# Kernel optimization log

Measured on AMD Instinct MI355X. Metric: run time of the kernel, lower is better.

The kernel has to match this reference:

```python
import jax, jax.numpy as jnp
import numpy as np

D_FEATURE = 1024
HEAD = 16
D_K = 64
D_V = 64
EPS = 1e-6


def setup_inputs() -> dict:
    key = jax.random.key(0)
    ks = jax.random.split(key, 12)
    B, S = 2, 2048
    s_in = 1.0 / np.sqrt(D_FEATURE)
    s_o = 1.0 / np.sqrt(HEAD * D_V)
    return {
        "q": jax.random.normal(ks[0], (B, S, D_FEATURE), jnp.float32),
        "k": jax.random.normal(ks[1], (B, S, D_FEATURE), jnp.float32),
        "v": jax.random.normal(ks[2], (B, S, D_FEATURE), jnp.float32),
        "Wq": jax.random.uniform(ks[3], (D_FEATURE, HEAD * D_K), jnp.float32, -s_in, s_in),
        "bq": jnp.zeros((HEAD * D_K,), jnp.float32),
        "Wk": jax.random.uniform(ks[4], (D_FEATURE, HEAD * D_K), jnp.float32, -s_in, s_in),
        "bk": jnp.zeros((HEAD * D_K,), jnp.float32),
        "Wv": jax.random.uniform(ks[5], (D_FEATURE, HEAD * D_V), jnp.float32, -s_in, s_in),
        "bv": jnp.zeros((HEAD * D_V,), jnp.float32),
        "Wo": jax.random.uniform(ks[6], (HEAD * D_V, D_FEATURE), jnp.float32, -s_o, s_o),
        "bo": jnp.zeros((D_FEATURE,), jnp.float32),
        "gamma": jnp.ones((D_FEATURE,), jnp.float32),
        "beta": jnp.zeros((D_FEATURE,), jnp.float32),
    }


def reference(q, k, v, Wq, bq, Wk, bk, Wv, bv, Wo, bo, gamma, beta):
    B, Sq, _ = q.shape
    Sk, Sv = k.shape[1], v.shape[1]
    shortcut = v
    # projections -> (b, h, s, d)
    qh = (q @ Wq + bq).reshape(B, Sq, HEAD, D_K).transpose(0, 2, 1, 3)
    kh = (k @ Wk + bk).reshape(B, Sk, HEAD, D_K).transpose(0, 2, 1, 3)
    vh = (v @ Wv + bv).reshape(B, Sv, HEAD, D_V).transpose(0, 2, 1, 3)
    scale = 1.0 / np.sqrt(D_K).astype(np.float32)
    scores = jnp.einsum('bhqd,bhkd->bhqk', qh * scale, kh)
    attn = jax.nn.softmax(scores, axis=-1)  # dropout is identity (p=0 / eval)
    ctx = jnp.einsum('bhqk,bhkd->bhqd', attn, vh)
    ctx = ctx.transpose(0, 2, 1, 3).reshape(B, Sv, HEAD * D_V)
    out = ctx @ Wo + bo
    out = out + shortcut
    # LayerNorm, eps=1e-6
    mu = out.mean(-1, keepdims=True)
    var = out.var(-1, keepdims=True)
    out = (out - mu) * jax.lax.rsqrt(var + EPS) * gamma + beta
    return out
```

## Files before the change

kernel.cpp:

```cpp
#include <hip/hip_runtime.h>

#define D_FEAT 1024
#define NTOK   4096
#define SEQ    2048
#define NHEAD  16
#define DK     64
#define QSCALE 0.1803368801111204f

typedef float          f32x4  __attribute__((ext_vector_type(4)));
typedef float          f32x16 __attribute__((ext_vector_type(16)));
typedef short          s16x8  __attribute__((ext_vector_type(8)));
typedef unsigned short u16x4  __attribute__((ext_vector_type(4)));

__device__ __forceinline__ unsigned short f2bf(float f) {
  union { float f; unsigned int u; } x; x.f = f;
  unsigned int r = x.u + 0x7fffu + ((x.u >> 16) & 1u);
  return (unsigned short)(r >> 16);
}
__device__ __forceinline__ unsigned short f2h(float f) {
  union { _Float16 h; unsigned short u; } x; x.h = (_Float16)f; return x.u;
}
__device__ __forceinline__ float h2f(unsigned short u) {
  union { _Float16 h; unsigned short u; } x; x.u = u; return (float)x.h;
}

__device__ __forceinline__ f32x4 mfma16(s16x8 a, s16x8 b, f32x4 c) {
  return __builtin_amdgcn_mfma_f32_16x16x32_bf16(a, b, c, 0, 0, 0);
}
__device__ __forceinline__ f32x16 mfma32(s16x8 a, s16x8 b, f32x16 c) {
  return __builtin_amdgcn_mfma_f32_32x32x16_bf16(a, b, c, 0, 0, 0);
}

__device__ __forceinline__ void gload16(const void* g, void* l) {
  __builtin_amdgcn_global_load_lds(
      (const __attribute__((address_space(1))) void*)g,
      (__attribute__((address_space(3))) void*)l, 16, 0, 0);
}

__global__ __launch_bounds__(256) void prep_kernel(
    const float* __restrict__ q, const float* __restrict__ k, const float* __restrict__ v,
    const float* __restrict__ Wq, const float* __restrict__ Wk,
    const float* __restrict__ Wv, const float* __restrict__ Wo,
    unsigned short* __restrict__ qb, unsigned short* __restrict__ kb,
    unsigned short* __restrict__ vb,
    unsigned short* __restrict__ WT, unsigned short* __restrict__ Wot)
{
  __shared__ float tile[32][33];
  const int bx = blockIdx.x, tid = threadIdx.x;
  if (bx < 12288) {
    int sel = bx >> 12;
    const float* src = sel == 0 ? q : (sel == 1 ? k : v);
    unsigned short* dst = sel == 0 ? qb : (sel == 1 ? kb : vb);
    size_t i = ((size_t)(bx & 4095) * 256 + tid) * 4;
    float4 f = *(const float4*)(src + i);
    u16x4 o; o.x = f2bf(f.x); o.y = f2bf(f.y); o.z = f2bf(f.z); o.w = f2bf(f.w);
    *(u16x4*)(dst + i) = o;
  } else {
    int t = bx - 12288;
    int z = t >> 10, rest = t & 1023;
    int bxt = rest & 31, byt = rest >> 5;
    const float* W = z == 0 ? Wq : z == 1 ? Wk : z == 2 ? Wv : Wo;
    unsigned short* T = (z < 3) ? (WT + (size_t)z * 1024 * 1024) : Wot;
    int tx = tid & 31, ty = tid >> 5;
    int n = bxt * 32 + tx;
    for (int i = 0; i < 4; ++i) {
      int kk = byt * 32 + ty + i * 8;
      tile[ty + i * 8][tx] = W[(size_t)kk * D_FEAT + n];
    }
    __syncthreads();
    int kk = byt * 32 + tx;
    for (int i = 0; i < 4; ++i) {
      int n2 = bxt * 32 + ty + i * 8;
      T[(size_t)n2 * D_FEAT + kk] = f2bf(tile[tx][ty + i * 8]);
    }
  }
}

__global__ __launch_bounds__(256, 3) void gemm_qkv(
    const unsigned short* __restrict__ qb, const unsigned short* __restrict__ kb,
    const unsigned short* __restrict__ vb, const unsigned short* __restrict__ WT,
    const float* __restrict__ bq, const float* __restrict__ bk, const float* __restrict__ bv,
    unsigned short* __restrict__ Qp, unsigned short* __restrict__ Kp, unsigned short* __restrict__ Vt)
{
  __shared__ __align__(16) unsigned short sAB[2 * 128 * 64];
  unsigned short* sA = sAB;
  unsigned short* sB = sAB + 128 * 64;
  const int tid = threadIdx.x;
  const int wave = tid >> 6, lane = tid & 63;
  const int quad = lane >> 4, l16 = lane & 15;
  const int wx = wave & 1, wy = wave >> 1;

  const int blk = blockIdx.x;
  const int xcd = blk & 7, jj = blk >> 3;
  const int chunk = jj >> 5;
  const int rest = jj & 31;
  const int n0i = rest & 7;
  const int by  = xcd * 4 + (rest >> 3);

  const unsigned short* rA;
  const unsigned short* rB;
  int m0, n0;
  if (chunk < 2) {
    m0 = by * 128; n0 = n0i * 128;
    rA = (chunk ? kb : qb) + (size_t)m0 * D_FEAT;
    rB = WT + (size_t)(chunk * 1024 + n0) * D_FEAT;
  } else {
    m0 = n0i * 128; n0 = by * 128;
    rA = WT + (size_t)(2048 + m0) * D_FEAT;
    rB = vb + (size_t)n0 * D_FEAT;
  }

  f32x4 acc[4][4];
  for (int mt = 0; mt < 4; ++mt)
    for (int nt = 0; nt < 4; ++nt) acc[mt][nt] = (f32x4){0.f, 0.f, 0.f, 0.f};

  const int rw8 = lane >> 3;
  const int cls = ((lane & 7) ^ (lane >> 3)) * 8;
  const int sw = l16 & 7;

  for (int k0 = 0; k0 < D_FEAT; k0 += 64) {
    __syncthreads();
    for (int j = 0; j < 4; ++j) {
      int ch = wave * 4 + j;
      gload16(rA + (size_t)(ch * 8 + rw8) * D_FEAT + k0 + cls, sA + ch * 512);
      gload16(rB + (size_t)(ch * 8 + rw8) * D_FEAT + k0 + cls, sB + ch * 512);
    }
    __syncthreads();
    s16x8 af[2][4], bfr[2][4];
    for (int kk = 0; kk < 2; ++kk) {
      int c = ((kk * 4 + quad) ^ sw) * 8;
      for (int mt = 0; mt < 4; ++mt)
        af[kk][mt] = *(const s16x8*)(sA + (wy * 64 + mt * 16 + l16) * 64 + c);
      for (int nt = 0; nt < 4; ++nt)
        bfr[kk][nt] = *(const s16x8*)(sB + (wx * 64 + nt * 16 + l16) * 64 + c);
    }
    for (int kk = 0; kk < 2; ++kk)
      for (int mt = 0; mt < 4; ++mt)
        for (int nt = 0; nt < 4; ++nt)
          acc[mt][nt] = mfma16(af[kk][mt], bfr[kk][nt], acc[mt][nt]);
  }

  if (chunk < 2) {
    const float* bias = chunk ? bk : bq;
    unsigned short* Cp = chunk ? Kp : Qp;
    const float scale = chunk == 0 ? QSCALE : 1.0f;
    for (int mt = 0; mt < 4; ++mt)
      for (int nt = 0; nt < 4; ++nt) {
        int col = n0 + wx * 64 + nt * 16 + l16;
        float bcol = bias[col];
        for (int r = 0; r < 4; ++r) {
          int row = m0 + wy * 64 + mt * 16 + quad * 4 + r;
          Cp[(size_t)row * D_FEAT + col] = f2bf((acc[mt][nt][r] + bcol) * scale);
        }
      }
  } else {
    for (int mt = 0; mt < 4; ++mt)
      for (int r = 0; r < 4; ++r) {
        float bfeat = bv[m0 + wy * 64 + mt * 16 + quad * 4 + r];
        for (int nt = 0; nt < 4; ++nt) acc[mt][nt][r] += bfeat;
      }
    unsigned short* tb = sAB;
    for (int p = 0; p < 2; ++p) {
      __syncthreads();
      if (wx == p) {
        for (int mt = 0; mt < 4; ++mt)
          for (int nt = 0; nt < 4; ++nt) {
            int tok_loc = nt * 16 + l16;
            for (int r = 0; r < 4; ++r) {
              int f_loc = wy * 64 + mt * 16 + quad * 4 + r;
              tb[f_loc * 72 + tok_loc] = f2bf(acc[mt][nt][r]);
            }
          }
      }
      __syncthreads();
      int n_base = n0 + p * 64;
      int b = n_base >> 11, tok0 = n_base & 2047;
      int ck = lane & 7;
      for (int j = 0; j < 4; ++j) {
        int f_loc = (wave * 4 + j) * 8 + rw8;
        int f = m0 + f_loc, hh = f >> 6, dv = f & 63;
        *(s16x8*)(Vt + ((size_t)(b * 16 + hh) * 64 + dv) * SEQ + tok0 + ck * 8) =
            *(const s16x8*)(tb + f_loc * 72 + ck * 8);
      }
    }
  }
}

__global__ __launch_bounds__(256) void gemm_o(
    const unsigned short* __restrict__ A, const unsigned short* __restrict__ Bt,
    const float* __restrict__ bias, const float* __restrict__ resid,
    float* __restrict__ Cout)
{
  __shared__ __align__(16) unsigned short sA[128 * 64];
  __shared__ __align__(16) unsigned short sB[64 * 64];
  const int tid = threadIdx.x;
  const int wave = tid >> 6, lane = tid & 63;
  const int quad = lane >> 4, l16 = lane & 15;
  const int wx = wave & 1, wy = wave >> 1;

  const int blk = blockIdx.x;
  const int xcd = blk & 7, jj = blk >> 3;
  const int n0 = (jj & 15) * 64;
  const int m0 = (xcd * 4 + (jj >> 4)) * 128;

  f32x4 acc[4][2];
  for (int mt = 0; mt < 4; ++mt)
    for (int nt = 0; nt < 2; ++nt) acc[mt][nt] = (f32x4){0.f, 0.f, 0.f, 0.f};

  const int rw8 = lane >> 3;
  const int cls = ((lane & 7) ^ (lane >> 3)) * 8;
  const int sw = l16 & 7;

  for (int k0 = 0; k0 < D_FEAT; k0 += 64) {
    __syncthreads();
    for (int j = 0; j < 4; ++j) {
      int ch = wave * 4 + j;
      gload16(A + (size_t)(m0 + ch * 8 + rw8) * D_FEAT + k0 + cls, sA + ch * 512);
    }
    for (int j = 0; j < 2; ++j) {
      int ch = wave * 2 + j;
      gload16(Bt + (size_t)(n0 + ch * 8 + rw8) * D_FEAT + k0 + cls, sB + ch * 512);
    }
    __syncthreads();
    s16x8 af[2][4], bfr[2][2];
    for (int kk = 0; kk < 2; ++kk) {
      int c = ((kk * 4 + quad) ^ sw) * 8;
      for (int mt = 0; mt < 4; ++mt)
        af[kk][mt] = *(const s16x8*)(sA + (wy * 64 + mt * 16 + l16) * 64 + c);
      for (int nt = 0; nt < 2; ++nt)
        bfr[kk][nt] = *(const s16x8*)(sB + (wx * 32 + nt * 16 + l16) * 64 + c);
    }
    for (int kk = 0; kk < 2; ++kk)
      for (int mt = 0; mt < 4; ++mt)
        for (int nt = 0; nt < 2; ++nt)
          acc[mt][nt] = mfma16(af[kk][mt], bfr[kk][nt], acc[mt][nt]);
  }

  for (int mt = 0; mt < 4; ++mt)
    for (int nt = 0; nt < 2; ++nt) {
      int col = n0 + wx * 32 + nt * 16 + l16;
      float bcol = bias[col];
      for (int r = 0; r < 4; ++r) {
        int row = m0 + wy * 64 + mt * 16 + quad * 4 + r;
        Cout[(size_t)row * D_FEAT + col] =
            acc[mt][nt][r] + bcol + resid[(size_t)row * D_FEAT + col];
      }
    }
}

__global__ __launch_bounds__(256, 4) void flash_part(
    const unsigned short* __restrict__ Qp,
    const unsigned short* __restrict__ Kp,
    const unsigned short* __restrict__ Vt,
    unsigned short* __restrict__ Opart,
    float* __restrict__ L)
{
  __shared__ __align__(16) unsigned short sQ[128 * 64];
  __shared__ __align__(16) unsigned short sK[64 * 64];
  __shared__ __align__(16) unsigned short sV[64 * 64];

  const int tid = threadIdx.x;
  const int wave = tid >> 6, lane = tid & 63;
  const int l32 = lane & 31, h = lane >> 5;

  const int blk = blockIdx.x;
  const int xcd = blk & 7, jj = blk >> 3;
  const int grp = xcd * 8 + (jj >> 4);
  const int q0 = (jj & 15) * 128;
  const int bh = grp & 31, z = grp >> 5;
  const int b = bh >> 4, hd = bh & 15;
  const int kbase = z * (SEQ / 2);
  const size_t base = (size_t)b * SEQ * D_FEAT + (size_t)hd * DK;
  const unsigned short* vt = Vt + (size_t)bh * 64 * SEQ;

  const int rw8 = lane >> 3;
  const int cls = ((lane & 7) ^ (lane >> 3)) * 8;

  for (int j = 0; j < 4; ++j) {
    int ch = wave * 4 + j;
    gload16(Qp + base + (size_t)(q0 + ch * 8 + rw8) * D_FEAT + cls, sQ + ch * 512);
  }
  __syncthreads();

  const int qrow = wave * 32 + l32;
  const int qsw = qrow & 7;
  s16x8 bq[4];
  for (int s = 0; s < 4; ++s)
    bq[s] = *(const s16x8*)(sQ + qrow * 64 + ((2 * s + h) ^ qsw) * 8);

  unsigned short* sP = sQ;

  f32x16 o0, o1;
  for (int r = 0; r < 16; ++r) { o0[r] = 0.f; o1[r] = 0.f; }
  float lsum = 0.f;

  const int ksw0 = l32 & 7;

  for (int k0 = kbase; k0 < kbase + SEQ / 2; k0 += 64) {
    __syncthreads();
    for (int j = 0; j < 2; ++j) {
      int ch = wave * 2 + j;
      gload16(Kp + base + (size_t)(k0 + ch * 8 + rw8) * D_FEAT + cls, sK + ch * 512);
      gload16(vt + (size_t)(ch * 8 + rw8) * SEQ + k0 + cls, sV + ch * 512);
    }
    __syncthreads();

    f32x16 st0, st1;
    for (int r = 0; r < 16; ++r) { st0[r] = 0.f; st1[r] = 0.f; }
    for (int s = 0; s < 4; ++s) {
      int csw = ((2 * s + h) ^ ksw0) * 8;
      s16x8 a0 = *(const s16x8*)(sK + l32 * 64 + csw);
      s16x8 a1 = *(const s16x8*)(sK + (32 + l32) * 64 + csw);
      st0 = mfma32(a0, bq[s], st0);
      st1 = mfma32(a1, bq[s], st1);
    }

    const int rowb = qrow * 64;
    for (int g = 0; g < 4; ++g) {
      unsigned int u[4];
      for (int r = 0; r < 4; ++r) {
        union { float f; unsigned int v; } x;
        x.f = __builtin_exp2f(st0[4 * g + r]);
        lsum += x.f; u[r] = x.v;
      }
      unsigned int w0 = __builtin_amdgcn_perm(u[1], u[0], 0x07060302u);
      unsigned int w1 = __builtin_amdgcn_perm(u[3], u[2], 0x07060302u);
      *(uint2*)(sP + rowb + ((g ^ qsw) * 8) + 4 * h) = make_uint2(w0, w1);
    }
    for (int g = 0; g < 4; ++g) {
      unsigned int u[4];
      for (int r = 0; r < 4; ++r) {
        union { float f; unsigned int v; } x;
        x.f = __builtin_exp2f(st1[4 * g + r]);
        lsum += x.f; u[r] = x.v;
      }
      unsigned int w0 = __builtin_amdgcn_perm(u[1], u[0], 0x07060302u);
      unsigned int w1 = __builtin_amdgcn_perm(u[3], u[2], 0x07060302u);
      *(uint2*)(sP + rowb + (((4 + g) ^ qsw) * 8) + 4 * h) = make_uint2(w0, w1);
    }

    s16x8 bp[4];
    for (int s = 0; s < 4; ++s)
      bp[s] = *(const s16x8*)(sP + rowb + ((2 * s + h) ^ qsw) * 8);

    for (int s = 0; s < 4; ++s) {
      int csw = ((2 * s + h) ^ ksw0) * 8;
      s16x8 a0 = *(const s16x8*)(sV + l32 * 64 + csw);
      s16x8 a1 = *(const s16x8*)(sV + (32 + l32) * 64 + csw);
      o0 = mfma32(a0, bp[s], o0);
      o1 = mfma32(a1, bp[s], o1);
    }
  }

  lsum += __shfl_xor(lsum, 32, 64);
  const size_t trow = (size_t)(z * 32 + bh) * SEQ + (q0 + qrow);
  unsigned short* orow = Opart + trow * 64;
  for (int g = 0; g < 4; ++g) {
    u16x4 ov;
    for (int r = 0; r < 4; ++r) ov[r] = f2h(o0[4 * g + r]);
    *(u16x4*)(orow + 8 * g + 4 * h) = ov;
  }
  for (int g = 0; g < 4; ++g) {
    u16x4 ov;
    for (int r = 0; r < 4; ++r) ov[r] = f2h(o1[4 * g + r]);
    *(u16x4*)(orow + 32 + 8 * g + 4 * h) = ov;
  }
  if (h == 0) L[trow] = lsum;
}

__global__ __launch_bounds__(256) void combine_kernel(
    const unsigned short* __restrict__ Opart, const float* __restrict__ L,
    unsigned short* __restrict__ ctx)
{
  const int idx = blockIdx.x * 256 + threadIdx.x;
  const int dq = idx & 15;
  const int trow = idx >> 4;
  const int bh = trow >> 11, tok = trow & 2047;
  const int b = bh >> 4, h = bh & 15;
  const int HS = 32 * SEQ;

  float inv = __builtin_amdgcn_rcpf(L[trow] + L[HS + trow]);

  u16x4 p0 = *(const u16x4*)(Opart + (size_t)trow * 64 + dq * 4);
  u16x4 p1 = *(const u16x4*)(Opart + ((size_t)HS + trow) * 64 + dq * 4);
  u16x4 o;
  for (int r = 0; r < 4; ++r)
    o[r] = f2bf((h2f(p0[r]) + h2f(p1[r])) * inv);
  *(u16x4*)(ctx + (size_t)b * SEQ * D_FEAT + (size_t)tok * D_FEAT + h * 64 + dq * 4) = o;
}

__global__ __launch_bounds__(256) void ln_kernel(
    const float* __restrict__ x, const float* __restrict__ gamma,
    const float* __restrict__ beta, float* __restrict__ out)
{
  const int row = blockIdx.x, tid = threadIdx.x;
  const int wave = tid >> 6, lane = tid & 63;
  const float* xr = x + (size_t)row * D_FEAT;
  float4 v = ((const float4*)xr)[tid];
  float s  = v.x + v.y + v.z + v.w;
  float ss = v.x * v.x + v.y * v.y + v.z * v.z + v.w * v.w;
  for (int off = 1; off < 64; off <<= 1) {
    s  += __shfl_xor(s,  off, 64);
    ss += __shfl_xor(ss, off, 64);
  }
  __shared__ float red[8];
  if (lane == 0) { red[wave] = s; red[wave + 4] = ss; }
  __syncthreads();
  s  = red[0] + red[1] + red[2] + red[3];
  ss = red[4] + red[5] + red[6] + red[7];
  float mean = s * (1.f / D_FEAT);
  float var  = ss * (1.f / D_FEAT) - mean * mean;
  float rstd = rsqrtf(var + 1e-6f);
  float4 g  = ((const float4*)gamma)[tid];
  float4 bt = ((const float4*)beta)[tid];
  float4 o;
  o.x = (v.x - mean) * rstd * g.x + bt.x;
  o.y = (v.y - mean) * rstd * g.y + bt.y;
  o.z = (v.z - mean) * rstd * g.z + bt.z;
  o.w = (v.w - mean) * rstd * g.w + bt.w;
  ((float4*)(out + (size_t)row * D_FEAT))[tid] = o;
}

extern "C" void kernel_launch(void* const* d_in, const int* in_sizes, int n_in,
                              void* d_out, int out_size, void* d_ws, size_t ws_size,
                              hipStream_t stream) {
  const float* q     = (const float*)d_in[0];
  const float* k     = (const float*)d_in[1];
  const float* v     = (const float*)d_in[2];
  const float* Wq    = (const float*)d_in[3];
  const float* bq    = (const float*)d_in[4];
  const float* Wk    = (const float*)d_in[5];
  const float* bk    = (const float*)d_in[6];
  const float* Wv    = (const float*)d_in[7];
  const float* bv    = (const float*)d_in[8];
  const float* Wo    = (const float*)d_in[9];
  const float* bo    = (const float*)d_in[10];
  const float* gamma = (const float*)d_in[11];
  const float* beta  = (const float*)d_in[12];

  char* w = (char*)d_ws;
  const size_t MB = 1u << 20;
  unsigned short* qb    = (unsigned short*)(w + 0 * MB);
  unsigned short* kb    = (unsigned short*)(w + 8 * MB);
  unsigned short* vb    = (unsigned short*)(w + 16 * MB);
  unsigned short* WT    = (unsigned short*)(w + 24 * MB);
  unsigned short* Wot   = (unsigned short*)(w + 30 * MB);
  unsigned short* Qp    = (unsigned short*)(w + 32 * MB);
  unsigned short* Kp    = (unsigned short*)(w + 40 * MB);
  unsigned short* Vt    = (unsigned short*)(w + 48 * MB);
  unsigned short* ctx   = (unsigned short*)(w + 56 * MB);
  float*          tmp   = (float*)(w + 64 * MB);
  unsigned short* Opart = (unsigned short*)(w + 0 * MB);
  float*          L     = (float*)(w + 16 * MB);

  prep_kernel<<<16384, 256, 0, stream>>>(q, k, v, Wq, Wk, Wv, Wo, qb, kb, vb, WT, Wot);

  gemm_qkv<<<768, 256, 0, stream>>>(qb, kb, vb, WT, bq, bk, bv, Qp, Kp, Vt);

  flash_part<<<1024, 256, 0, stream>>>(Qp, Kp, Vt, Opart, L);

  combine_kernel<<<4096, 256, 0, stream>>>(Opart, L, ctx);

  gemm_o<<<512, 256, 0, stream>>>(ctx, Wot, bo, v, tmp);

  ln_kernel<<<NTOK, 256, 0, stream>>>(tmp, gamma, beta, (float*)d_out);
}
```

Before: 246.4 us.

## Fuse all six stages into one persistent kernel with grid barriers

Replaces six separate launches (prep, QKV GEMM, flash attention, combine, output GEMM, LayerNorm) with a single persistent kernel of 1024 blocks. The stages are separated by atomic-counter grid barriers. The aim is to remove per-launch overhead and inter-kernel gaps. The costs are idle blocks in stages that use fewer than 1024 blocks, and a forward-progress requirement that all 1024 blocks be co-resident (occupancy hint of 4 per CU). Buffer offsets are reused (tmp now aliases Qp/Kp), and the weight transpose store is vectorised.

```diff
diff --git a/kernel.cpp b/kernel.cpp
--- a/kernel.cpp
+++ b/kernel.cpp
@@ -6,6 +6,7 @@
 #define NHEAD  16
 #define DK     64
 #define QSCALE 0.1803368801111204f
+#define GRID   1024
 
 typedef float          f32x4  __attribute__((ext_vector_type(4)));
 typedef float          f32x16 __attribute__((ext_vector_type(16)));
@@ -37,388 +38,373 @@
       (__attribute__((address_space(3))) void*)l, 16, 0, 0);
 }
 
-__global__ __launch_bounds__(256) void prep_kernel(
+__device__ __forceinline__ void gbar(unsigned* cnt, unsigned target) {
+  __syncthreads();
+  if (threadIdx.x == 0) {
+    __threadfence();
+    atomicAdd(cnt, 1u);
+    while (atomicAdd(cnt, 0u) < target) __builtin_amdgcn_s_sleep(2);
+    __threadfence();
+  }
+  __syncthreads();
+}
+
+__global__ __launch_bounds__(256, 4) void mega_kernel(
     const float* __restrict__ q, const float* __restrict__ k, const float* __restrict__ v,
     const float* __restrict__ Wq, const float* __restrict__ Wk,
     const float* __restrict__ Wv, const float* __restrict__ Wo,
-    unsigned short* __restrict__ qb, unsigned short* __restrict__ kb,
-    unsigned short* __restrict__ vb,
-    unsigned short* __restrict__ WT, unsigned short* __restrict__ Wot)
+    const float* __restrict__ bq, const float* __restrict__ bk,
+    const float* __restrict__ bv, const float* __restrict__ bo,
+    const float* __restrict__ gamma, const float* __restrict__ beta,
+    unsigned short* qb, unsigned short* kb, unsigned short* vb,
+    unsigned short* WT, unsigned short* Wot,
+    unsigned short* Qp, unsigned short* Kp, unsigned short* Vt,
+    unsigned short* Opart, float* L, unsigned short* ctx, float* tmp,
+    float* out, unsigned* bar)
 {
-  __shared__ float tile[32][33];
-  const int bx = blockIdx.x, tid = threadIdx.x;
-  if (bx < 12288) {
-    int sel = bx >> 12;
-    const float* src = sel == 0 ? q : (sel == 1 ? k : v);
-    unsigned short* dst = sel == 0 ? qb : (sel == 1 ? kb : vb);
-    size_t i = ((size_t)(bx & 4095) * 256 + tid) * 4;
-    float4 f = *(const float4*)(src + i);
-    u16x4 o; o.x = f2bf(f.x); o.y = f2bf(f.y); o.z = f2bf(f.z); o.w = f2bf(f.w);
-    *(u16x4*)(dst + i) = o;
-  } else {
-    int t = bx - 12288;
-    int z = t >> 10, rest = t & 1023;
-    int bxt = rest & 31, byt = rest >> 5;
-    const float* W = z == 0 ? Wq : z == 1 ? Wk : z == 2 ? Wv : Wo;
-    unsigned short* T = (z < 3) ? (WT + (size_t)z * 1024 * 1024) : Wot;
-    int tx = tid & 31, ty = tid >> 5;
-    int n = bxt * 32 + tx;
-    for (int i = 0; i < 4; ++i) {
-      int kk = byt * 32 + ty + i * 8;
-      tile[ty + i * 8][tx] = W[(size_t)kk * D_FEAT + n];
-    }
-    __syncthreads();
-    int kk = byt * 32 + tx;
-    for (int i = 0; i < 4; ++i) {
-      int n2 = bxt * 32 + ty + i * 8;
-      T[(size_t)n2 * D_FEAT + kk] = f2bf(tile[tx][ty + i * 8]);
-    }
-  }
-}
-
-__global__ __launch_bounds__(256, 3) void gemm_qkv(
-    const unsigned short* __restrict__ qb, const unsigned short* __restrict__ kb,
-    const unsigned short* __restrict__ vb, const unsigned short* __restrict__ WT,
-    const float* __restrict__ bq, const float* __restrict__ bk, const float* __restrict__ bv,
-    unsigned short* __restrict__ Qp, unsigned short* __restrict__ Kp, unsigned short* __restrict__ Vt)
-{
-  __shared__ __align__(16) unsigned short sAB[2 * 128 * 64];
-  unsigned short* sA = sAB;
-  unsigned short* sB = sAB + 128 * 64;
+  __shared__ __align__(16) unsigned char smem[32768];
   const int tid = threadIdx.x;
+  const int blk = blockIdx.x;
   const int wave = tid >> 6, lane = tid & 63;
   const int quad = lane >> 4, l16 = lane & 15;
-  const int wx = wave & 1, wy = wave >> 1;
-
-  const int blk = blockIdx.x;
-  const int xcd = blk & 7, jj = blk >> 3;
-  const int chunk = jj >> 5;
-  const int rest = jj & 31;
-  const int n0i = rest & 7;
-  const int by  = xcd * 4 + (rest >> 3);
-
-  const unsigned short* rA;
-  const unsigned short* rB;
-  int m0, n0;
-  if (chunk < 2) {
-    m0 = by * 128; n0 = n0i * 128;
-    rA = (chunk ? kb : qb) + (size_t)m0 * D_FEAT;
-    rB = WT + (size_t)(chunk * 1024 + n0) * D_FEAT;
-  } else {
-    m0 = n0i * 128; n0 = by * 128;
-    rA = WT + (size_t)(2048 + m0) * D_FEAT;
-    rB = vb + (size_t)n0 * D_FEAT;
-  }
-
-  f32x4 acc[4][4];
-  for (int mt = 0; mt < 4; ++mt)
-    for (int nt = 0; nt < 4; ++nt) acc[mt][nt] = (f32x4){0.f, 0.f, 0.f, 0.f};
-
   const int rw8 = lane >> 3;
   const int cls = ((lane & 7) ^ (lane >> 3)) * 8;
-  const int sw = l16 & 7;
-
-  for (int k0 = 0; k0 < D_FEAT; k0 += 64) {
-    __syncthreads();
+
+  {
+    float (*tile)[33] = (float(*)[33])smem;
+    for (int u = blk; u < 16384; u += GRID) {
+      if (u < 12288) {
+        int sel = u >> 12;
+        const float* src = sel == 0 ? q : (sel == 1 ? k : v);
+        unsigned short* dst = sel == 0 ? qb : (sel == 1 ? kb : vb);
+        size_t i = ((size_t)(u & 4095) * 256 + tid) * 4;
+        float4 f = *(const float4*)(src + i);
+        u16x4 o; o.x = f2bf(f.x); o.y = f2bf(f.y); o.z = f2bf(f.z); o.w = f2bf(f.w);
+        *(u16x4*)(dst + i) = o;
+      } else {
+        int t = u - 12288;
+        int z = t >> 10, rest = t & 1023;
+        int bxt = rest & 31, byt = rest >> 5;
+        const float* W = z == 0 ? Wq : z == 1 ? Wk : z == 2 ? Wv : Wo;
+        unsigned short* T = (z < 3) ? (WT + (size_t)z * 1024 * 1024) : Wot;
+        int tx = tid & 31, ty = tid >> 5;
+        for (int i2 = 0; i2 < 4; ++i2)
+          tile[ty + i2 * 8][tx] =
+              W[(size_t)(byt * 32 + ty + i2 * 8) * D_FEAT + bxt * 32 + tx];
+        __syncthreads();
+        int n_loc = tid >> 3, kc = (tid & 7) * 4;
+        u16x4 ovv;
+        for (int j = 0; j < 4; ++j) ovv[j] = f2bf(tile[kc + j][n_loc]);
+        *(u16x4*)(T + (size_t)(bxt * 32 + n_loc) * D_FEAT + byt * 32 + kc) = ovv;
+        __syncthreads();
+      }
+    }
+  }
+  gbar(bar, 1 * GRID);
+
+  if (blk < 768) {
+    unsigned short* sA = (unsigned short*)smem;
+    unsigned short* sB = (unsigned short*)smem + 128 * 64;
+    const int wx = wave & 1, wy = wave >> 1;
+    const int xcd = blk & 7, jj = blk >> 3;
+    const int chunk = jj >> 5;
+    const int rest = jj & 31;
+    const int n0i = rest & 7;
+    const int by  = xcd * 4 + (rest >> 3);
+
+    const unsigned short* rA;
+    const unsigned short* rB;
+    int m0, n0;
+    if (chunk < 2) {
+      m0 = by * 128; n0 = n0i * 128;
+      rA = (chunk ? kb : qb) + (size_t)m0 * D_FEAT;
+      rB = WT + (size_t)(chunk * 1024 + n0) * D_FEAT;
+    } else {
+      m0 = n0i * 128; n0 = by * 128;
+      rA = WT + (size_t)(2048 + m0) * D_FEAT;
+      rB = vb + (size_t)n0 * D_FEAT;
+    }
+
+    f32x4 acc[4][4];
+    for (int mt = 0; mt < 4; ++mt)
+      for (int nt = 0; nt < 4; ++nt) acc[mt][nt] = (f32x4){0.f, 0.f, 0.f, 0.f};
+
+    const int sw = l16 & 7;
+    for (int k0 = 0; k0 < D_FEAT; k0 += 64) {
+      __syncthreads();
+      for (int j = 0; j < 4; ++j) {
+        int ch = wave * 4 + j;
+        gload16(rA + (size_t)(ch * 8 + rw8) * D_FEAT + k0 + cls, sA + ch * 512);
+        gload16(rB + (size_t)(ch * 8 + rw8) * D_FEAT + k0 + cls, sB + ch * 512);
+      }
+      __syncthreads();
+      for (int kk = 0; kk < 2; ++kk) {
+        int c = ((kk * 4 + quad) ^ sw) * 8;
+        s16x8 af[4], bfr[4];
+        for (int mt = 0; mt < 4; ++mt)
+          af[mt] = *(const s16x8*)(sA + (wy * 64 + mt * 16 + l16) * 64 + c);
+        for (int nt = 0; nt < 4; ++nt)
+          bfr[nt] = *(const s16x8*)(sB + (wx * 64 + nt * 16 + l16) * 64 + c);
+        for (int mt = 0; mt < 4; ++mt)
+          for (int nt = 0; nt < 4; ++nt)
+            acc[mt][nt] = mfma16(af[mt], bfr[nt], acc[mt][nt]);
+      }
+    }
+
+    if (chunk < 2) {
+      const float* bias = chunk ? bk : bq;
+      unsigned short* Cp = chunk ? Kp : Qp;
+      const float scale = chunk == 0 ? QSCALE : 1.0f;
+      for (int mt = 0; mt < 4; ++mt)
+        for (int nt = 0; nt < 4; ++nt) {
+          int col = n0 + wx * 64 + nt * 16 + l16;
+          float bcol = bias[col];
+          for (int r = 0; r < 4; ++r) {
+            int row = m0 + wy * 64 + mt * 16 + quad * 4 + r;
+            Cp[(size_t)row * D_FEAT + col] = f2bf((acc[mt][nt][r] + bcol) * scale);
+          }
+        }
+    } else {
+      for (int mt = 0; mt < 4; ++mt)
+        for (int r = 0; r < 4; ++r) {
+          float bfeat = bv[m0 + wy * 64 + mt * 16 + quad * 4 + r];
+          for (int nt = 0; nt < 4; ++nt) acc[mt][nt][r] += bfeat;
+        }
+      unsigned short* tb = (unsigned short*)smem;
+      for (int p = 0; p < 2; ++p) {
+        __syncthreads();
+        if (wx == p) {
+          for (int mt = 0; mt < 4; ++mt)
+            for (int nt = 0; nt < 4; ++nt) {
+              int tok_loc = nt * 16 + l16;
+              for (int r = 0; r < 4; ++r) {
+                int f_loc = wy * 64 + mt * 16 + quad * 4 + r;
+                tb[f_loc * 72 + tok_loc] = f2bf(acc[mt][nt][r]);
+              }
+            }
+        }
+        __syncthreads();
+        int n_base = n0 + p * 64;
+        int b = n_base >> 11, tok0 = n_base & 2047;
+        int ck = lane & 7;
+        for (int j = 0; j < 4; ++j) {
+          int f_loc = (wave * 4 + j) * 8 + rw8;
+          int f = m0 + f_loc, hh = f >> 6, dv = f & 63;
+          *(s16x8*)(Vt + ((size_t)(b * 16 + hh) * 64 + dv) * SEQ + tok0 + ck * 8) =
+              *(const s16x8*)(tb + f_loc * 72 + ck * 8);
+        }
+      }
+    }
+  }
+  gbar(bar, 2 * GRID);
+
+  {
+    unsigned short* sQ = (unsigned short*)smem;
+    unsigned short* sK = sQ + 128 * 64;
+    unsigned short* sV = sK + 64 * 64;
+    const int l32 = lane & 31, h = lane >> 5;
+
+    const int xcd = blk & 7, jj = blk >> 3;
+    const int grp = xcd * 8 + (jj >> 4);
+    const int q0 = (jj & 15) * 128;
+    const int bh = grp & 31, z = grp >> 5;
+    const int b = bh >> 4, hd = bh & 15;
+    const int kbase = z * (SEQ / 2);
+    const size_t base = (size_t)b * SEQ * D_FEAT + (size_t)hd * DK;
+    const unsigned short* vt = Vt + (size_t)bh * 64 * SEQ;
+
     for (int j = 0; j < 4; ++j) {
       int ch = wave * 4 + j;
-      gload16(rA + (size_t)(ch * 8 + rw8) * D_FEAT + k0 + cls, sA + ch * 512);
-      gload16(rB + (size_t)(ch * 8 + rw8) * D_FEAT + k0 + cls, sB + ch * 512);
+      gload16(Qp + base + (size_t)(q0 + ch * 8 + rw8) * D_FEAT + cls, sQ + ch * 512);
     }
     __syncthreads();
-    s16x8 af[2][4], bfr[2][4];
-    for (int kk = 0; kk < 2; ++kk) {
-      int c = ((kk * 4 + quad) ^ sw) * 8;
-      for (int mt = 0; mt < 4; ++mt)
-        af[kk][mt] = *(const s16x8*)(sA + (wy * 64 + mt * 16 + l16) * 64 + c);
-      for (int nt = 0; nt < 4; ++nt)
-        bfr[kk][nt] = *(const s16x8*)(sB + (wx * 64 + nt * 16 + l16) * 64 + c);
-    }
-    for (int kk = 0; kk < 2; ++kk)
-      for (int mt = 0; mt < 4; ++mt)
-        for (int nt = 0; nt < 4; ++nt)
-          acc[mt][nt] = mfma16(af[kk][mt], bfr[kk][nt], acc[mt][nt]);
-  }
-
-  if (chunk < 2) {
-    const float* bias = chunk ? bk : bq;
-    unsigned short* Cp = chunk ? Kp : Qp;
-    const float scale = chunk == 0 ? QSCALE : 1.0f;
+
+    const int qrow = wave * 32 + l32;
+    const int qsw = qrow & 7;
+    s16x8 bqf[4];
+    for (int s = 0; s < 4; ++s)
+      bqf[s] = *(const s16x8*)(sQ + qrow * 64 + ((2 * s + h) ^ qsw) * 8);
+
+    unsigned short* sP = sQ;
+
+    f32x16 o0, o1;
+    for (int r = 0; r < 16; ++r) { o0[r] = 0.f; o1[r] = 0.f; }
+    float lsum = 0.f;
+    const int ksw0 = l32 & 7;
+
+    for (int k0 = kbase; k0 < kbase + SEQ / 2; k0 += 64) {
+      __syncthreads();
+      for (int j = 0; j < 2; ++j) {
+        int ch = wave * 2 + j;
+        gload16(Kp + base + (size_t)(k0 + ch * 8 + rw8) * D_FEAT + cls, sK + ch * 512);
+        gload16(vt + (size_t)(ch * 8 + rw8) * SEQ + k0 + cls, sV + ch * 512);
+      }
+      __syncthreads();
+
+      f32x16 st0, st1;
+      for (int r = 0; r < 16; ++r) { st0[r] = 0.f; st1[r] = 0.f; }
+      for (int s = 0; s < 4; ++s) {
+        int csw = ((2 * s + h) ^ ksw0) * 8;
+        s16x8 a0 = *(const s16x8*)(sK + l32 * 64 + csw);
+        s16x8 a1 = *(const s16x8*)(sK + (32 + l32) * 64 + csw);
+        st0 = mfma32(a0, bqf[s], st0);
+        st1 = mfma32(a1, bqf[s], st1);
+      }
+
+      const int rowb = qrow * 64;
+      for (int g = 0; g < 4; ++g) {
+        unsigned int u[4];
+        for (int r = 0; r < 4; ++r) {
+          union { float f; unsigned int v; } x;
+          x.f = __builtin_exp2f(st0[4 * g + r]);
+          lsum += x.f; u[r] = x.v;
+        }
+        unsigned int w0 = __builtin_amdgcn_perm(u[1], u[0], 0x07060302u);
+        unsigned int w1 = __builtin_amdgcn_perm(u[3], u[2], 0x07060302u);
+        *(uint2*)(sP + rowb + ((g ^ qsw) * 8) + 4 * h) = make_uint2(w0, w1);
+      }
+      for (int g = 0; g < 4; ++g) {
+        unsigned int u[4];
+        for (int r = 0; r < 4; ++r) {
+          union { float f; unsigned int v; } x;
+          x.f = __builtin_exp2f(st1[4 * g + r]);
+          lsum += x.f; u[r] = x.v;
+        }
+        unsigned int w0 = __builtin_amdgcn_perm(u[1], u[0], 0x07060302u);
+        unsigned int w1 = __builtin_amdgcn_perm(u[3], u[2], 0x07060302u);
+        *(uint2*)(sP + rowb + (((4 + g) ^ qsw) * 8) + 4 * h) = make_uint2(w0, w1);
+      }
+
+      s16x8 bp[4];
+      for (int s = 0; s < 4; ++s)
+        bp[s] = *(const s16x8*)(sP + rowb + ((2 * s + h) ^ qsw) * 8);
+
+      for (int s = 0; s < 4; ++s) {
+        int csw = ((2 * s + h) ^ ksw0) * 8;
+        s16x8 a0 = *(const s16x8*)(sV + l32 * 64 + csw);
+        s16x8 a1 = *(const s16x8*)(sV + (32 + l32) * 64 + csw);
+        o0 = mfma32(a0, bp[s], o0);
+        o1 = mfma32(a1, bp[s], o1);
+      }
+    }
+
+    lsum += __shfl_xor(lsum, 32, 64);
+    const size_t trow = (size_t)(z * 32 + bh) * SEQ + (q0 + qrow);
+    unsigned short* orow = Opart + trow * 64;
+    for (int g = 0; g < 4; ++g) {
+      u16x4 ov;
+      for (int r = 0; r < 4; ++r) ov[r] = f2h(o0[4 * g + r]);
+      *(u16x4*)(orow + 8 * g + 4 * h) = ov;
+    }
+    for (int g = 0; g < 4; ++g) {
+      u16x4 ov;
+      for (int r = 0; r < 4; ++r) ov[r] = f2h(o1[4 * g + r]);
+      *(u16x4*)(orow + 32 + 8 * g + 4 * h) = ov;
+    }
+    if (h == 0) L[trow] = lsum;
+  }
+  gbar(bar, 3 * GRID);
+
+  {
+    const int HS = 32 * SEQ;
+    for (int i = 0; i < 4; ++i) {
+      int idx = (blk + GRID * i) * 256 + tid;
+      int dq = idx & 15;
+      int trow = idx >> 4;
+      int bh = trow >> 11, tok = trow & 2047;
+      int b = bh >> 4, h = bh & 15;
+      float inv = __builtin_amdgcn_rcpf(L[trow] + L[HS + trow]);
+      u16x4 p0 = *(const u16x4*)(Opart + (size_t)trow * 64 + dq * 4);
+      u16x4 p1 = *(const u16x4*)(Opart + ((size_t)HS + trow) * 64 + dq * 4);
+      u16x4 o;
+      for (int r = 0; r < 4; ++r)
+        o[r] = f2bf((h2f(p0[r]) + h2f(p1[r])) * inv);
+      *(u16x4*)(ctx + (size_t)b * SEQ * D_FEAT + (size_t)tok * D_FEAT +
+                h * 64 + dq * 4) = o;
+    }
+  }
+  gbar(bar, 4 * GRID);
+
+  if (blk < 512) {
+    unsigned short* sA = (unsigned short*)smem;
+    unsigned short* sB = (unsigned short*)smem + 128 * 64;
+    const int wx = wave & 1, wy = wave >> 1;
+    const int xcd = blk & 7, jj = blk >> 3;
+    const int n0 = (jj & 15) * 64;
+    const int m0 = (xcd * 4 + (jj >> 4)) * 128;
+
+    f32x4 acc[4][2];
     for (int mt = 0; mt < 4; ++mt)
-      for (int nt = 0; nt < 4; ++nt) {
-        int col = n0 + wx * 64 + nt * 16 + l16;
-        float bcol = bias[col];
+      for (int nt = 0; nt < 2; ++nt) acc[mt][nt] = (f32x4){0.f, 0.f, 0.f, 0.f};
+
+    const int sw = l16 & 7;
+    for (int k0 = 0; k0 < D_FEAT; k0 += 64) {
+      __syncthreads();
+      for (int j = 0; j < 4; ++j) {
+        int ch = wave * 4 + j;
+        gload16(ctx + (size_t)(m0 + ch * 8 + rw8) * D_FEAT + k0 + cls, sA + ch * 512);
+      }
+      for (int j = 0; j < 2; ++j) {
+        int ch = wave * 2 + j;
+        gload16(Wot + (size_t)(n0 + ch * 8 + rw8) * D_FEAT + k0 + cls, sB + ch * 512);
+      }
+      __syncthreads();
+      for (int kk = 0; kk < 2; ++kk) {
+        int c = ((kk * 4 + quad) ^ sw) * 8;
+        s16x8 af[4], bfr[2];
+        for (int mt = 0; mt < 4; ++mt)
+          af[mt] = *(const s16x8*)(sA + (wy * 64 + mt * 16 + l16) * 64 + c);
+        for (int nt = 0; nt < 2; ++nt)
+          bfr[nt] = *(const s16x8*)(sB + (wx * 32 + nt * 16 + l16) * 64 + c);
+        for (int mt = 0; mt < 4; ++mt)
+          for (int nt = 0; nt < 2; ++nt)
+            acc[mt][nt] = mfma16(af[mt], bfr[nt], acc[mt][nt]);
+      }
+    }
+
+    for (int mt = 0; mt < 4; ++mt)
+      for (int nt = 0; nt < 2; ++nt) {
+        int col = n0 + wx * 32 + nt * 16 + l16;
+        float bcol = bo[col];
         for (int r = 0; r < 4; ++r) {
           int row = m0 + wy * 64 + mt * 16 + quad * 4 + r;
-          Cp[(size_t)row * D_FEAT + col] = f2bf((acc[mt][nt][r] + bcol) * scale);
-        }
-      }
-  } else {
-    for (int mt = 0; mt < 4; ++mt)
-      for (int r = 0; r < 4; ++r) {
-        float bfeat = bv[m0 + wy * 64 + mt * 16 + quad * 4 + r];
-        for (int nt = 0; nt < 4; ++nt) acc[mt][nt][r] += bfeat;
-      }
-    unsigned short* tb = sAB;
-    for (int p = 0; p < 2; ++p) {
-      __syncthreads();
-      if (wx == p) {
-        for (int mt = 0; mt < 4; ++mt)
-          for (int nt = 0; nt < 4; ++nt) {
-            int tok_loc = nt * 16 + l16;
-            for (int r = 0; r < 4; ++r) {
-              int f_loc = wy * 64 + mt * 16 + quad * 4 + r;
-              tb[f_loc * 72 + tok_loc] = f2bf(acc[mt][nt][r]);
-            }
-          }
-      }
-      __syncthreads();
-      int n_base = n0 + p * 64;
-      int b = n_base >> 11, tok0 = n_base & 2047;
-      int ck = lane & 7;
-      for (int j = 0; j < 4; ++j) {
-        int f_loc = (wave * 4 + j) * 8 + rw8;
-        int f = m0 + f_loc, hh = f >> 6, dv = f & 63;
-        *(s16x8*)(Vt + ((size_t)(b * 16 + hh) * 64 + dv) * SEQ + tok0 + ck * 8) =
-            *(const s16x8*)(tb + f_loc * 72 + ck * 8);
-      }
-    }
-  }
-}
-
-__global__ __launch_bounds__(256) void gemm_o(
-    const unsigned short* __restrict__ A, const unsigned short* __restrict__ Bt,
-    const float* __restrict__ bias, const float* __restrict__ resid,
-    float* __restrict__ Cout)
-{
-  __shared__ __align__(16) unsigned short sA[128 * 64];
-  __shared__ __align__(16) unsigned short sB[64 * 64];
-  const int tid = threadIdx.x;
-  const int wave = tid >> 6, lane = tid & 63;
-  const int quad = lane >> 4, l16 = lane & 15;
-  const int wx = wave & 1, wy = wave >> 1;
-
-  const int blk = blockIdx.x;
-  const int xcd = blk & 7, jj = blk >> 3;
-  const int n0 = (jj & 15) * 64;
-  const int m0 = (xcd * 4 + (jj >> 4)) * 128;
-
-  f32x4 acc[4][2];
-  for (int mt = 0; mt < 4; ++mt)
-    for (int nt = 0; nt < 2; ++nt) acc[mt][nt] = (f32x4){0.f, 0.f, 0.f, 0.f};
-
-  const int rw8 = lane >> 3;
-  const int cls = ((lane & 7) ^ (lane >> 3)) * 8;
-  const int sw = l16 & 7;
-
-  for (int k0 = 0; k0 < D_FEAT; k0 += 64) {
-    __syncthreads();
-    for (int j = 0; j < 4; ++j) {
-      int ch = wave * 4 + j;
-      gload16(A + (size_t)(m0 + ch * 8 + rw8) * D_FEAT + k0 + cls, sA + ch * 512);
-    }
-    for (int j = 0; j < 2; ++j) {
-      int ch = wave * 2 + j;
-      gload16(Bt + (size_t)(n0 + ch * 8 + rw8) * D_FEAT + k0 + cls, sB + ch * 512);
-    }
-    __syncthreads();
-    s16x8 af[2][4], bfr[2][2];
-    for (int kk = 0; kk < 2; ++kk) {
-      int c = ((kk * 4 + quad) ^ sw) * 8;
-      for (int mt = 0; mt < 4; ++mt)
-        af[kk][mt] = *(const s16x8*)(sA + (wy * 64 + mt * 16 + l16) * 64 + c);
-      for (int nt = 0; nt < 2; ++nt)
-        bfr[kk][nt] = *(const s16x8*)(sB + (wx * 32 + nt * 16 + l16) * 64 + c);
-    }
-    for (int kk = 0; kk < 2; ++kk)
-      for (int mt = 0; mt < 4; ++mt)
-        for (int nt = 0; nt < 2; ++nt)
-          acc[mt][nt] = mfma16(af[kk][mt], bfr[kk][nt], acc[mt][nt]);
-  }
-
-  for (int mt = 0; mt < 4; ++mt)
-    for (int nt = 0; nt < 2; ++nt) {
-      int col = n0 + wx * 32 + nt * 16 + l16;
-      float bcol = bias[col];
-      for (int r = 0; r < 4; ++r) {
-        int row = m0 + wy * 64 + mt * 16 + quad * 4 + r;
-        Cout[(size_t)row * D_FEAT + col] =
-            acc[mt][nt][r] + bcol + resid[(size_t)row * D_FEAT + col];
-      }
-    }
-}
-
-__global__ __launch_bounds__(256, 4) void flash_part(
-    const unsigned short* __restrict__ Qp,
-    const unsigned short* __restrict__ Kp,
-    const unsigned short* __restrict__ Vt,
-    unsigned short* __restrict__ Opart,
-    float* __restrict__ L)
-{
-  __shared__ __align__(16) unsigned short sQ[128 * 64];
-  __shared__ __align__(16) unsigned short sK[64 * 64];
-  __shared__ __align__(16) unsigned short sV[64 * 64];
-
-  const int tid = threadIdx.x;
-  const int wave = tid >> 6, lane = tid & 63;
-  const int l32 = lane & 31, h = lane >> 5;
-
-  const int blk = blockIdx.x;
-  const int xcd = blk & 7, jj = blk >> 3;
-  const int grp = xcd * 8 + (jj >> 4);
-  const int q0 = (jj & 15) * 128;
-  const int bh = grp & 31, z = grp >> 5;
-  const int b = bh >> 4, hd = bh & 15;
-  const int kbase = z * (SEQ / 2);
-  const size_t base = (size_t)b * SEQ * D_FEAT + (size_t)hd * DK;
-  const unsigned short* vt = Vt + (size_t)bh * 64 * SEQ;
-
-  const int rw8 = lane >> 3;
-  const int cls = ((lane & 7) ^ (lane >> 3)) * 8;
-
-  for (int j = 0; j < 4; ++j) {
-    int ch = wave * 4 + j;
-    gload16(Qp + base + (size_t)(q0 + ch * 8 + rw8) * D_FEAT + cls, sQ + ch * 512);
-  }
-  __syncthreads();
-
-  const int qrow = wave * 32 + l32;
-  const int qsw = qrow & 7;
-  s16x8 bq[4];
-  for (int s = 0; s < 4; ++s)
-    bq[s] = *(const s16x8*)(sQ + qrow * 64 + ((2 * s + h) ^ qsw) * 8);
-
-  unsigned short* sP = sQ;
-
-  f32x16 o0, o1;
-  for (int r = 0; r < 16; ++r) { o0[r] = 0.f; o1[r] = 0.f; }
-  float lsum = 0.f;
-
-  const int ksw0 = l32 & 7;
-
-  for (int k0 = kbase; k0 < kbase + SEQ / 2; k0 += 64) {
-    __syncthreads();
-    for (int j = 0; j < 2; ++j) {
-      int ch = wave * 2 + j;
-      gload16(Kp + base + (size_t)(k0 + ch * 8 + rw8) * D_FEAT + cls, sK + ch * 512);
-      gload16(vt + (size_t)(ch * 8 + rw8) * SEQ + k0 + cls, sV + ch * 512);
-    }
-    __syncthreads();
-
-    f32x16 st0, st1;
-    for (int r = 0; r < 16; ++r) { st0[r] = 0.f; st1[r] = 0.f; }
-    for (int s = 0; s < 4; ++s) {
-      int csw = ((2 * s + h) ^ ksw0) * 8;
-      s16x8 a0 = *(const s16x8*)(sK + l32 * 64 + csw);
-      s16x8 a1 = *(const s16x8*)(sK + (32 + l32) * 64 + csw);
-      st0 = mfma32(a0, bq[s], st0);
-      st1 = mfma32(a1, bq[s], st1);
-    }
-
-    const int rowb = qrow * 64;
-    for (int g = 0; g < 4; ++g) {
-      unsigned int u[4];
-      for (int r = 0; r < 4; ++r) {
-        union { float f; unsigned int v; } x;
-        x.f = __builtin_exp2f(st0[4 * g + r]);
-        lsum += x.f; u[r] = x.v;
-      }
-      unsigned int w0 = __builtin_amdgcn_perm(u[1], u[0], 0x07060302u);
-      unsigned int w1 = __builtin_amdgcn_perm(u[3], u[2], 0x07060302u);
-      *(uint2*)(sP + rowb + ((g ^ qsw) * 8) + 4 * h) = make_uint2(w0, w1);
-    }
-    for (int g = 0; g < 4; ++g) {
-      unsigned int u[4];
-      for (int r = 0; r < 4; ++r) {
-        union { float f; unsigned int v; } x;
-        x.f = __builtin_exp2f(st1[4 * g + r]);
-        lsum += x.f; u[r] = x.v;
-      }
-      unsigned int w0 = __builtin_amdgcn_perm(u[1], u[0], 0x07060302u);
-      unsigned int w1 = __builtin_amdgcn_perm(u[3], u[2], 0x07060302u);
-      *(uint2*)(sP + rowb + (((4 + g) ^ qsw) * 8) + 4 * h) = make_uint2(w0, w1);
-    }
-
-    s16x8 bp[4];
-    for (int s = 0; s < 4; ++s)
-      bp[s] = *(const s16x8*)(sP + rowb + ((2 * s + h) ^ qsw) * 8);
-
-    for (int s = 0; s < 4; ++s) {
-      int csw = ((2 * s + h) ^ ksw0) * 8;
-      s16x8 a0 = *(const s16x8*)(sV + l32 * 64 + csw);
-      s16x8 a1 = *(const s16x8*)(sV + (32 + l32) * 64 + csw);
-      o0 = mfma32(a0, bp[s], o0);
-      o1 = mfma32(a1, bp[s], o1);
-    }
-  }
-
-  lsum += __shfl_xor(lsum, 32, 64);
-  const size_t trow = (size_t)(z * 32 + bh) * SEQ + (q0 + qrow);
-  unsigned short* orow = Opart + trow * 64;
-  for (int g = 0; g < 4; ++g) {
-    u16x4 ov;
-    for (int r = 0; r < 4; ++r) ov[r] = f2h(o0[4 * g + r]);
-    *(u16x4*)(orow + 8 * g + 4 * h) = ov;
-  }
-  for (int g = 0; g < 4; ++g) {
-    u16x4 ov;
-    for (int r = 0; r < 4; ++r) ov[r] = f2h(o1[4 * g + r]);
-    *(u16x4*)(orow + 32 + 8 * g + 4 * h) = ov;
-  }
-  if (h == 0) L[trow] = lsum;
-}
-
-__global__ __launch_bounds__(256) void combine_kernel(
-    const unsigned short* __restrict__ Opart, const float* __restrict__ L,
-    unsigned short* __restrict__ ctx)
-{
-  const int idx = blockIdx.x * 256 + threadIdx.x;
-  const int dq = idx & 15;
-  const int trow = idx >> 4;
-  const int bh = trow >> 11, tok = trow & 2047;
-  const int b = bh >> 4, h = bh & 15;
-  const int HS = 32 * SEQ;
-
-  float inv = __builtin_amdgcn_rcpf(L[trow] + L[HS + trow]);
-
-  u16x4 p0 = *(const u16x4*)(Opart + (size_t)trow * 64 + dq * 4);
-  u16x4 p1 = *(const u16x4*)(Opart + ((size_t)HS + trow) * 64 + dq * 4);
-  u16x4 o;
-  for (int r = 0; r < 4; ++r)
-    o[r] = f2bf((h2f(p0[r]) + h2f(p1[r])) * inv);
-  *(u16x4*)(ctx + (size_t)b * SEQ * D_FEAT + (size_t)tok * D_FEAT + h * 64 + dq * 4) = o;
-}
-
-__global__ __launch_bounds__(256) void ln_kernel(
-    const float* __restrict__ x, const float* __restrict__ gamma,
-    const float* __restrict__ beta, float* __restrict__ out)
-{
-  const int row = blockIdx.x, tid = threadIdx.x;
-  const int wave = tid >> 6, lane = tid & 63;
-  const float* xr = x + (size_t)row * D_FEAT;
-  float4 v = ((const float4*)xr)[tid];
-  float s  = v.x + v.y + v.z + v.w;
-  float ss = v.x * v.x + v.y * v.y + v.z * v.z + v.w * v.w;
-  for (int off = 1; off < 64; off <<= 1) {
-    s  += __shfl_xor(s,  off, 64);
-    ss += __shfl_xor(ss, off, 64);
-  }
-  __shared__ float red[8];
-  if (lane == 0) { red[wave] = s; red[wave + 4] = ss; }
-  __syncthreads();
-  s  = red[0] + red[1] + red[2] + red[3];
-  ss = red[4] + red[5] + red[6] + red[7];
-  float mean = s * (1.f / D_FEAT);
-  float var  = ss * (1.f / D_FEAT) - mean * mean;
-  float rstd = rsqrtf(var + 1e-6f);
-  float4 g  = ((const float4*)gamma)[tid];
-  float4 bt = ((const float4*)beta)[tid];
-  float4 o;
-  o.x = (v.x - mean) * rstd * g.x + bt.x;
-  o.y = (v.y - mean) * rstd * g.y + bt.y;
-  o.z = (v.z - mean) * rstd * g.z + bt.z;
-  o.w = (v.w - mean) * rstd * g.w + bt.w;
-  ((float4*)(out + (size_t)row * D_FEAT))[tid] = o;
+          tmp[(size_t)row * D_FEAT + col] =
+              acc[mt][nt][r] + bcol + v[(size_t)row * D_FEAT + col];
+        }
+      }
+  }
+  gbar(bar, 5 * GRID);
+
+  {
+    float* red = (float*)smem;
+    for (int i = 0; i < 4; ++i) {
+      int row = blk * 4 + i;
+      const float* xr = tmp + (size_t)row * D_FEAT;
+      float4 vv = ((const float4*)xr)[tid];
+      float s  = vv.x + vv.y + vv.z + vv.w;
+      float ss = vv.x * vv.x + vv.y * vv.y + vv.z * vv.z + vv.w * vv.w;
+      for (int off = 1; off < 64; off <<= 1) {
+        s  += __shfl_xor(s,  off, 64);
+        ss += __shfl_xor(ss, off, 64);
+      }
+      if (lane == 0) { red[wave] = s; red[wave + 4] = ss; }
+      __syncthreads();
+      s  = red[0] + red[1] + red[2] + red[3];
+      ss = red[4] + red[5] + red[6] + red[7];
+      float mean = s * (1.f / D_FEAT);
+      float var  = ss * (1.f / D_FEAT) - mean * mean;
+      float rstd = rsqrtf(var + 1e-6f);
+      float4 g  = ((const float4*)gamma)[tid];
+      float4 bt = ((const float4*)beta)[tid];
+      float4 o;
+      o.x = (vv.x - mean) * rstd * g.x + bt.x;
+      o.y = (vv.y - mean) * rstd * g.y + bt.y;
+      o.z = (vv.z - mean) * rstd * g.z + bt.z;
+      o.w = (vv.w - mean) * rstd * g.w + bt.w;
+      ((float4*)(out + (size_t)row * D_FEAT))[tid] = o;
+      __syncthreads();
+    }
+  }
 }
 
 extern "C" void kernel_launch(void* const* d_in, const int* in_sizes, int n_in,
@@ -449,19 +435,15 @@
   unsigned short* Kp    = (unsigned short*)(w + 40 * MB);
   unsigned short* Vt    = (unsigned short*)(w + 48 * MB);
   unsigned short* ctx   = (unsigned short*)(w + 56 * MB);
-  float*          tmp   = (float*)(w + 64 * MB);
   unsigned short* Opart = (unsigned short*)(w + 0 * MB);
   float*          L     = (float*)(w + 16 * MB);
-
-  prep_kernel<<<16384, 256, 0, stream>>>(q, k, v, Wq, Wk, Wv, Wo, qb, kb, vb, WT, Wot);
-
-  gemm_qkv<<<768, 256, 0, stream>>>(qb, kb, vb, WT, bq, bk, bv, Qp, Kp, Vt);
-
-  flash_part<<<1024, 256, 0, stream>>>(Qp, Kp, Vt, Opart, L);
-
-  combine_kernel<<<4096, 256, 0, stream>>>(Opart, L, ctx);
-
-  gemm_o<<<512, 256, 0, stream>>>(ctx, Wot, bo, v, tmp);
-
-  ln_kernel<<<NTOK, 256, 0, stream>>>(tmp, gamma, beta, (float*)d_out);
-}
+  float*          tmp   = (float*)(w + 32 * MB);
+  unsigned*       bar   = (unsigned*)(w + 64 * MB);
+
+  hipMemsetAsync(bar, 0, 64, stream);
+
+  mega_kernel<<<GRID, 256, 0, stream>>>(
+      q, k, v, Wq, Wk, Wv, Wo, bq, bk, bv, bo, gamma, beta,
+      qb, kb, vb, WT, Wot, Qp, Kp, Vt, Opart, L, ctx, tmp,
+      (float*)d_out, bar);
+}
```

New measurement: 879.6 us. 257% more time.
